# Performance work log

Hardware: AMD Instinct MI355X
Metric: run time of the kernel (lower is better)

## Reference

```python
import jax, jax.numpy as jnp
import numpy as np
from jax import lax

B, N = 4, 32768          # clouds, points per cloud (offsets are equal-sized)
CIN, COUT, S = 128, 256, 2048  # in_channels, out_channels, num_samples
EPS = 1e-5               # BatchNorm eps


def fps(xyz, npoint=S):
    """Farthest point sampling over xyz [N,3]; deterministic start index 0.
    Mirrors the torch loop: record current farthest, update min-distance, argmax."""
    n = xyz.shape[0]

    def step(carry, _):
        distance, farthest = carry
        centroid = xyz[farthest]                       # [3]
        dist = jnp.sum((xyz - centroid) ** 2, axis=1)  # [N]
        distance = jnp.minimum(distance, dist)
        new_farthest = jnp.argmax(distance).astype(jnp.int32)
        return (distance, new_farthest), farthest

    init = (jnp.full((n,), 1e10, dtype=xyz.dtype), jnp.int32(0))
    _, centroids = lax.scan(step, init, None, length=npoint)
    return centroids  # [npoint] int32


def setup_inputs():
    key = jax.random.key(0)
    k1, k2, k3 = jax.random.split(key, 3)
    coord = jax.random.normal(k1, (B * N, 3), dtype=jnp.float32)
    feat = jax.random.normal(k2, (B * N, CIN), dtype=jnp.float32)
    offset = (jnp.arange(1, B + 1, dtype=jnp.int32)) * N  # cumulative counts
    W = jax.random.normal(k3, (COUT, CIN), dtype=jnp.float32) / np.sqrt(CIN)
    gamma = jnp.ones((COUT,), dtype=jnp.float32)
    beta = jnp.zeros((COUT,), dtype=jnp.float32)
    return {"coord": coord, "feat": feat, "offset": offset,
            "W": W, "gamma": gamma, "beta": beta}


def reference(coord, feat, offset, W, gamma, beta):
    # fc -> PointBatchNorm (training-mode batch stats over B*N rows) -> ReLU
    x = feat @ W.T                                  # [B*N, COUT]
    mean = jnp.mean(x, axis=0)
    var = jnp.mean((x - mean) ** 2, axis=0)         # biased var, as torch BN
    x = (x - mean) * lax.rsqrt(var + EPS) * gamma + beta
    x = jax.nn.relu(x)

    coord_b = coord.reshape(B, N, 3)
    feat_b = x.reshape(B, N, COUT)
    idx = jax.vmap(fps)(coord_b)                    # [B, S] int32

    new_coords = jnp.take_along_axis(coord_b, idx[..., None], axis=1).reshape(B * S, 3)
    new_feats = jnp.take_along_axis(feat_b, idx[..., None], axis=1).reshape(B * S, COUT)
    new_offsets = jnp.arange(1, B + 1, dtype=jnp.int32) * S
    return new_coords, new_feats, new_offsets
```

## Files before the change

kernel.cpp:

```cpp
#include <hip/hip_runtime.h>

#define NB 4
#define NPT 32768
#define QPT 8192
#define CIN 128
#define COUT 256
#define NS 2048
#define THR 512
#define PPT 16

#define WS_G 0
#define WS_FSUM 16384
#define WS_SLOT 16512
#define WS_GSCALE 16576
#define WS_GBIAS 16832
#define WS_IDX 17088

#define OUT_COORD 0
#define OUT_FEAT 24576
#define OUT_OFFS 2121728

__global__ __launch_bounds__(THR) void fused1(
    const float* __restrict__ coord, const float* __restrict__ feat,
    float* __restrict__ wsf, int* __restrict__ wsi,
    unsigned long long* __restrict__ slots)
{
  __shared__ unsigned long long s_key[2];
  __shared__ float s_fs[4][128];

  const int bid = blockIdx.x;
  const int t = threadIdx.x;
  const bool is_fps = (bid < 32) && ((bid & 7) < 4);

  if (is_fps) {
    const int cl = bid & 3;
    const int h = bid >> 3;
    const int gbase = h * QPT;
    const float* xyz = coord + (size_t)cl * NPT * 3;
    int* idx_out = wsi + cl * NS;
    unsigned long long* slot = slots + cl * 8;

    float px[PPT], py[PPT], pz[PPT], dv[PPT];
#pragma unroll
    for (int j = 0; j < PPT; ++j) {
      int p = gbase + j * THR + t;
      px[j] = xyz[p * 3 + 0];
      py[j] = xyz[p * 3 + 1];
      pz[j] = xyz[p * 3 + 2];
      dv[j] = 1e10f;
    }
    if (t == 0) {
      if (h == 0) idx_out[0] = 0;
      s_key[0] = s_key[1] = 0ull;
    }
    float cx = xyz[0], cy = xyz[1], cz = xyz[2];
    __syncthreads();

    const int lane = t & 63;
    for (int it = 1; it < NS; ++it) {
      const int par = it & 1;
      const unsigned long long utag = (unsigned long long)it;
      float bd = -1.f;
      int bj = 0;
#pragma unroll
      for (int j = 0; j < PPT; ++j) {
        float dx = px[j] - cx, dy = py[j] - cy, dz = pz[j] - cz;
        float sx = dx * dx, sy = dy * dy, sz = dz * dz;
        asm volatile("" : "+v"(sx), "+v"(sy), "+v"(sz));
        float nd = fminf(dv[j], (sx + sy) + sz);
        dv[j] = nd;
        if (nd > bd) { bd = nd; bj = j; }
      }
      const int gidx = gbase + bj * THR + t;
      const unsigned long long tkey =
          (utag << 48) |
          ((unsigned long long)(unsigned)__float_as_int(bd) << 15) |
          (unsigned)(32767 - gidx);
      unsigned long long wkey = tkey;
#pragma unroll
      for (int o = 32; o > 0; o >>= 1) {
        unsigned long long ok = __shfl_xor(wkey, o, 64);
        wkey = ok > wkey ? ok : wkey;
      }
      if (lane == 0) atomicMax(&s_key[par], wkey);
      __syncthreads();
      const unsigned long long skey = s_key[par];
      if (tkey == skey)
        __hip_atomic_store(&slot[par * 4 + h], skey,
                           __ATOMIC_RELAXED, __HIP_MEMORY_SCOPE_AGENT);
      unsigned long long v0, v1, v2, v3;
      do {
        v0 = __hip_atomic_load(&slot[par * 4 + 0],
                               __ATOMIC_RELAXED, __HIP_MEMORY_SCOPE_AGENT);
        v1 = __hip_atomic_load(&slot[par * 4 + 1],
                               __ATOMIC_RELAXED, __HIP_MEMORY_SCOPE_AGENT);
        v2 = __hip_atomic_load(&slot[par * 4 + 2],
                               __ATOMIC_RELAXED, __HIP_MEMORY_SCOPE_AGENT);
        v3 = __hip_atomic_load(&slot[par * 4 + 3],
                               __ATOMIC_RELAXED, __HIP_MEMORY_SCOPE_AGENT);
      } while ((v0 >> 48) != utag || (v1 >> 48) != utag ||
               (v2 >> 48) != utag || (v3 >> 48) != utag);
      const unsigned long long b01 = v0 > v1 ? v0 : v1;
      const unsigned long long b23 = v2 > v3 ? v2 : v3;
      const unsigned long long best = b01 > b23 ? b01 : b23;
      const int widx = 32767 - (int)(best & 0x7fff);
      if (h == 0 && t == 0) idx_out[it] = widx;
      cx = xyz[widx * 3 + 0];
      cy = xyz[widx * 3 + 1];
      cz = xyz[widx * 3 + 2];
    }
  } else {
    const int g = (bid < 32) ? ((bid >> 3) * 4 + (bid & 7) - 4) : (bid - 16);
    if (g < 128) {
      const float* fr = feat + (size_t)g * 1024 * CIN;
      const int ti = (t & 31) * 4;
      const int tj = (t >> 5) * 8;
      float acc[4][8];
#pragma unroll
      for (int a = 0; a < 4; ++a)
#pragma unroll
        for (int b2 = 0; b2 < 8; ++b2) acc[a][b2] = 0.f;
#pragma unroll 4
      for (int r = 0; r < 1024; ++r) {
        const float* rowp = fr + r * CIN;
        float4 a4 = *(const float4*)(rowp + ti);
        float4 b4 = *(const float4*)(rowp + tj);
        float4 b5 = *(const float4*)(rowp + tj + 4);
        float av[4] = {a4.x, a4.y, a4.z, a4.w};
        float bv[8] = {b4.x, b4.y, b4.z, b4.w, b5.x, b5.y, b5.z, b5.w};
#pragma unroll
        for (int a = 0; a < 4; ++a)
#pragma unroll
          for (int b2 = 0; b2 < 8; ++b2) acc[a][b2] += av[a] * bv[b2];
      }
      float* G = wsf + WS_G;
#pragma unroll
      for (int a = 0; a < 4; ++a)
#pragma unroll
        for (int b2 = 0; b2 < 8; ++b2)
          atomicAdd(&G[(ti + a) * CIN + (tj + b2)], acc[a][b2]);
    } else {
      const int fb = g - 128;
      const size_t base = (size_t)fb * 16384;
      const int c = t & 127, rg = t >> 7;
      float s = 0.f;
      for (int r = rg; r < 16384; r += 4)
        s += feat[(base + r) * CIN + c];
      s_fs[rg][c] = s;
      __syncthreads();
      if (t < 128) {
        float v = s_fs[0][t] + s_fs[1][t] + s_fs[2][t] + s_fs[3][t];
        atomicAdd(&wsf[WS_FSUM + t], v);
      }
    }
  }
}

__global__ __launch_bounds__(128) void finalize_k(
    const float* __restrict__ W, const float* __restrict__ gamma,
    const float* __restrict__ beta, float* __restrict__ wsf)
{
  const int c = blockIdx.x, i = threadIdx.x;
  const float* G = wsf + WS_G;
  const float* fsum = wsf + WS_FSUM;
  const float* Gi = G + i * CIN;
  const float* Wc = W + c * CIN;
  float td = 0.f;
#pragma unroll 8
  for (int j = 0; j < CIN; j += 4) {
    float4 g4 = *(const float4*)(Gi + j);
    float4 w4 = *(const float4*)(Wc + j);
    td += g4.x * w4.x + g4.y * w4.y + g4.z * w4.z + g4.w * w4.w;
  }
  const float wci = Wc[i];
  float q = wci * td;
  float m = fsum[i] * wci;
#pragma unroll
  for (int o = 32; o > 0; o >>= 1) {
    q += __shfl_xor(q, o, 64);
    m += __shfl_xor(m, o, 64);
  }
  __shared__ float sq[2], sm[2];
  if ((i & 63) == 0) { sq[i >> 6] = q; sm[i >> 6] = m; }
  __syncthreads();
  if (i == 0) {
    const float inv_m = 1.f / 131072.f;
    float mean = (sm[0] + sm[1]) * inv_m;
    float e2 = (sq[0] + sq[1]) * inv_m;
    float var = e2 - mean * mean;
    float rstd = rsqrtf(var + 1e-5f);
    float gs = gamma[c] * rstd;
    wsf[WS_GSCALE + c] = gs;
    wsf[WS_GBIAS + c] = beta[c] - mean * gs;
  }
}

__global__ __launch_bounds__(256) void gather_k(
    const float* __restrict__ coord, const float* __restrict__ feat,
    const float* __restrict__ W, const float* __restrict__ wsf,
    const int* __restrict__ wsi, float* __restrict__ out)
{
  const int p = blockIdx.x, t = threadIdx.x;
  const int b = p >> 11;
  const int idx = wsi[p];
  const size_t row = (size_t)b * NPT + idx;
  __shared__ float lf[CIN];
  if (t < CIN) lf[t] = feat[row * CIN + t];
  __syncthreads();
  const float* Wc = W + t * CIN;
  float acc = 0.f;
#pragma unroll 8
  for (int k = 0; k < CIN; k += 4) {
    float4 w4 = *(const float4*)(Wc + k);
    acc += lf[k] * w4.x + lf[k + 1] * w4.y + lf[k + 2] * w4.z + lf[k + 3] * w4.w;
  }
  float y = fmaxf(fmaf(acc, wsf[WS_GSCALE + t], wsf[WS_GBIAS + t]), 0.f);
  out[OUT_FEAT + (size_t)p * COUT + t] = y;
  if (t < 3) out[OUT_COORD + p * 3 + t] = coord[row * 3 + t];
  if (p == 0 && t < 4) out[OUT_OFFS + t] = (float)((t + 1) * NS);
}

extern "C" void kernel_launch(void* const* d_in, const int* in_sizes, int n_in,
                              void* d_out, int out_size, void* d_ws, size_t ws_size,
                              hipStream_t stream)
{
  const float* coord = (const float*)d_in[0];
  const float* feat  = (const float*)d_in[1];
  const float* W     = (const float*)d_in[3];
  const float* gamma = (const float*)d_in[4];
  const float* beta  = (const float*)d_in[5];
  float* wsf = (float*)d_ws;
  int* wsi = (int*)(wsf + WS_IDX);
  unsigned long long* slots = (unsigned long long*)(wsf + WS_SLOT);
  float* out = (float*)d_out;

  hipMemsetAsync(d_ws, 0, (WS_SLOT + 64) * sizeof(float), stream);

  fused1<<<152, THR, 0, stream>>>(coord, feat, wsf, wsi, slots);
  finalize_k<<<COUT, 128, 0, stream>>>(W, gamma, beta, wsf);
  gather_k<<<NB * NS, 256, 0, stream>>>(coord, feat, W, wsf, wsi, out);
}
```

Before: 4.746 ms.

## Split FPS per cloud across two 1024-thread blocks instead of four

Each cloud's farthest-point sampling now runs on two blocks of 1024 threads, each holding half the points, instead of four blocks of 512. The per-iteration cross-block handshake polls one partner slot rather than four, which should cut global-memory spin latency on every sampling step. The GEMM and column-sum side blocks are resized to 1024 threads so the work split still matches. In exchange, each block's intra-block reduction and __syncthreads span twice as many waves, and the grid drops to 80 blocks.

```diff
diff --git a/kernel.cpp b/kernel.cpp
--- a/kernel.cpp
+++ b/kernel.cpp
@@ -2,11 +2,11 @@
 
 #define NB 4
 #define NPT 32768
-#define QPT 8192
+#define HPT 16384
 #define CIN 128
 #define COUT 256
 #define NS 2048
-#define THR 512
+#define THR 1024
 #define PPT 16
 
 #define WS_G 0
@@ -26,19 +26,19 @@
     unsigned long long* __restrict__ slots)
 {
   __shared__ unsigned long long s_key[2];
-  __shared__ float s_fs[4][128];
+  __shared__ float s_fs[8][128];
 
   const int bid = blockIdx.x;
   const int t = threadIdx.x;
-  const bool is_fps = (bid < 32) && ((bid & 7) < 4);
+  const bool is_fps = (bid < 12) && ((bid & 7) < 4);
 
   if (is_fps) {
     const int cl = bid & 3;
     const int h = bid >> 3;
-    const int gbase = h * QPT;
+    const int gbase = h * HPT;
     const float* xyz = coord + (size_t)cl * NPT * 3;
     int* idx_out = wsi + cl * NS;
-    unsigned long long* slot = slots + cl * 8;
+    unsigned long long* slot = slots + cl * 4;
 
     float px[PPT], py[PPT], pz[PPT], dv[PPT];
 #pragma unroll
@@ -86,23 +86,14 @@
       __syncthreads();
       const unsigned long long skey = s_key[par];
       if (tkey == skey)
-        __hip_atomic_store(&slot[par * 4 + h], skey,
+        __hip_atomic_store(&slot[par * 2 + h], skey,
                            __ATOMIC_RELAXED, __HIP_MEMORY_SCOPE_AGENT);
-      unsigned long long v0, v1, v2, v3;
+      unsigned long long v;
       do {
-        v0 = __hip_atomic_load(&slot[par * 4 + 0],
-                               __ATOMIC_RELAXED, __HIP_MEMORY_SCOPE_AGENT);
-        v1 = __hip_atomic_load(&slot[par * 4 + 1],
-                               __ATOMIC_RELAXED, __HIP_MEMORY_SCOPE_AGENT);
-        v2 = __hip_atomic_load(&slot[par * 4 + 2],
-                               __ATOMIC_RELAXED, __HIP_MEMORY_SCOPE_AGENT);
-        v3 = __hip_atomic_load(&slot[par * 4 + 3],
-                               __ATOMIC_RELAXED, __HIP_MEMORY_SCOPE_AGENT);
-      } while ((v0 >> 48) != utag || (v1 >> 48) != utag ||
-               (v2 >> 48) != utag || (v3 >> 48) != utag);
-      const unsigned long long b01 = v0 > v1 ? v0 : v1;
-      const unsigned long long b23 = v2 > v3 ? v2 : v3;
-      const unsigned long long best = b01 > b23 ? b01 : b23;
+        v = __hip_atomic_load(&slot[par * 2 + (1 - h)],
+                              __ATOMIC_RELAXED, __HIP_MEMORY_SCOPE_AGENT);
+      } while ((v >> 48) != utag);
+      const unsigned long long best = v > skey ? v : skey;
       const int widx = 32767 - (int)(best & 0x7fff);
       if (h == 0 && t == 0) idx_out[it] = widx;
       cx = xyz[widx * 3 + 0];
@@ -110,11 +101,12 @@
       cz = xyz[widx * 3 + 2];
     }
   } else {
-    const int g = (bid < 32) ? ((bid >> 3) * 4 + (bid & 7) - 4) : (bid - 16);
-    if (g < 128) {
-      const float* fr = feat + (size_t)g * 1024 * CIN;
-      const int ti = (t & 31) * 4;
-      const int tj = (t >> 5) * 8;
+    const int g = (bid < 8) ? (bid - 4) : (bid - 8);
+    if (g < 64) {
+      const int tt = t & 511, sub = t >> 9;
+      const float* fr = feat + ((size_t)g * 2048 + sub * 1024) * CIN;
+      const int ti = (tt & 31) * 4;
+      const int tj = (tt >> 5) * 8;
       float acc[4][8];
 #pragma unroll
       for (int a = 0; a < 4; ++a)
@@ -140,16 +132,17 @@
         for (int b2 = 0; b2 < 8; ++b2)
           atomicAdd(&G[(ti + a) * CIN + (tj + b2)], acc[a][b2]);
     } else {
-      const int fb = g - 128;
+      const int fb = g - 64;
       const size_t base = (size_t)fb * 16384;
       const int c = t & 127, rg = t >> 7;
       float s = 0.f;
-      for (int r = rg; r < 16384; r += 4)
+      for (int r = rg; r < 16384; r += 8)
         s += feat[(base + r) * CIN + c];
       s_fs[rg][c] = s;
       __syncthreads();
       if (t < 128) {
-        float v = s_fs[0][t] + s_fs[1][t] + s_fs[2][t] + s_fs[3][t];
+        float v = s_fs[0][t] + s_fs[1][t] + s_fs[2][t] + s_fs[3][t] +
+                  s_fs[4][t] + s_fs[5][t] + s_fs[6][t] + s_fs[7][t];
         atomicAdd(&wsf[WS_FSUM + t], v);
       }
     }
@@ -236,7 +229,7 @@
 
   hipMemsetAsync(d_ws, 0, (WS_SLOT + 64) * sizeof(float), stream);
 
-  fused1<<<152, THR, 0, stream>>>(coord, feat, wsf, wsi, slots);
+  fused1<<<80, THR, 0, stream>>>(coord, feat, wsf, wsi, slots);
   finalize_k<<<COUT, 128, 0, stream>>>(W, gamma, beta, wsf);
   gather_k<<<NB * NS, 256, 0, stream>>>(coord, feat, W, wsf, wsi, out);
 }
```

Measured after the change: 5.091 ms. 1.07x slower.

## Replace per-block LDS reduction with per-wave global slots in FPS

Applied to the files above, without the earlier changes.

Each FPS iteration now skips the block-level shared atomicMax and __syncthreads. Every wave instead publishes its own best key to one of 32 global slots per cloud. Each wave then polls all 32 slots at once, using one lane per slot and a wave vote, and reduces them with shuffles. This removes one barrier per iteration from the serial 2047-step loop, at the cost of more global polling traffic. The shared array is also enlarged to 64KB, which probably limits occupancy or co-residency of the blocks.

```diff
diff --git a/kernel.cpp b/kernel.cpp
--- a/kernel.cpp
+++ b/kernel.cpp
@@ -12,9 +12,9 @@
 #define WS_G 0
 #define WS_FSUM 16384
 #define WS_SLOT 16512
-#define WS_GSCALE 16576
-#define WS_GBIAS 16832
-#define WS_IDX 17088
+#define WS_GSCALE 17024
+#define WS_GBIAS 17280
+#define WS_IDX 17536
 
 #define OUT_COORD 0
 #define OUT_FEAT 24576
@@ -25,9 +25,7 @@
     float* __restrict__ wsf, int* __restrict__ wsi,
     unsigned long long* __restrict__ slots)
 {
-  __shared__ unsigned long long s_key[2];
-  __shared__ float s_fs[4][128];
-
+  __shared__ float smem[16384];
   const int bid = blockIdx.x;
   const int t = threadIdx.x;
   const bool is_fps = (bid < 32) && ((bid & 7) < 4);
@@ -38,7 +36,7 @@
     const int gbase = h * QPT;
     const float* xyz = coord + (size_t)cl * NPT * 3;
     int* idx_out = wsi + cl * NS;
-    unsigned long long* slot = slots + cl * 8;
+    unsigned long long* slot = slots + cl * 64;
 
     float px[PPT], py[PPT], pz[PPT], dv[PPT];
 #pragma unroll
@@ -49,17 +47,15 @@
       pz[j] = xyz[p * 3 + 2];
       dv[j] = 1e10f;
     }
-    if (t == 0) {
-      if (h == 0) idx_out[0] = 0;
-      s_key[0] = s_key[1] = 0ull;
-    }
+    if (h == 0 && t == 0) idx_out[0] = 0;
     float cx = xyz[0], cy = xyz[1], cz = xyz[2];
-    __syncthreads();
-
     const int lane = t & 63;
+    const int wslot = h * 8 + (t >> 6);
+
     for (int it = 1; it < NS; ++it) {
       const int par = it & 1;
       const unsigned long long utag = (unsigned long long)it;
+      unsigned long long* slotp = slot + par * 32;
       float bd = -1.f;
       int bj = 0;
 #pragma unroll
@@ -72,38 +68,29 @@
         if (nd > bd) { bd = nd; bj = j; }
       }
       const int gidx = gbase + bj * THR + t;
-      const unsigned long long tkey =
+      unsigned long long wkey =
           (utag << 48) |
           ((unsigned long long)(unsigned)__float_as_int(bd) << 15) |
           (unsigned)(32767 - gidx);
-      unsigned long long wkey = tkey;
 #pragma unroll
       for (int o = 32; o > 0; o >>= 1) {
         unsigned long long ok = __shfl_xor(wkey, o, 64);
         wkey = ok > wkey ? ok : wkey;
       }
-      if (lane == 0) atomicMax(&s_key[par], wkey);
-      __syncthreads();
-      const unsigned long long skey = s_key[par];
-      if (tkey == skey)
-        __hip_atomic_store(&slot[par * 4 + h], skey,
+      if (lane == 0)
+        __hip_atomic_store(&slotp[wslot], wkey,
                            __ATOMIC_RELAXED, __HIP_MEMORY_SCOPE_AGENT);
-      unsigned long long v0, v1, v2, v3;
+      unsigned long long v;
       do {
-        v0 = __hip_atomic_load(&slot[par * 4 + 0],
-                               __ATOMIC_RELAXED, __HIP_MEMORY_SCOPE_AGENT);
-        v1 = __hip_atomic_load(&slot[par * 4 + 1],
-                               __ATOMIC_RELAXED, __HIP_MEMORY_SCOPE_AGENT);
-        v2 = __hip_atomic_load(&slot[par * 4 + 2],
-                               __ATOMIC_RELAXED, __HIP_MEMORY_SCOPE_AGENT);
-        v3 = __hip_atomic_load(&slot[par * 4 + 3],
-                               __ATOMIC_RELAXED, __HIP_MEMORY_SCOPE_AGENT);
-      } while ((v0 >> 48) != utag || (v1 >> 48) != utag ||
-               (v2 >> 48) != utag || (v3 >> 48) != utag);
-      const unsigned long long b01 = v0 > v1 ? v0 : v1;
-      const unsigned long long b23 = v2 > v3 ? v2 : v3;
-      const unsigned long long best = b01 > b23 ? b01 : b23;
-      const int widx = 32767 - (int)(best & 0x7fff);
+        v = __hip_atomic_load(&slotp[lane & 31],
+                              __ATOMIC_RELAXED, __HIP_MEMORY_SCOPE_AGENT);
+      } while (!__all((int)((v >> 48) == utag)));
+#pragma unroll
+      for (int o = 16; o > 0; o >>= 1) {
+        unsigned long long ov = __shfl_xor(v, o, 64);
+        v = ov > v ? ov : v;
+      }
+      const int widx = 32767 - (int)(v & 0x7fff);
       if (h == 0 && t == 0) idx_out[it] = widx;
       cx = xyz[widx * 3 + 0];
       cy = xyz[widx * 3 + 1];
@@ -140,6 +127,7 @@
         for (int b2 = 0; b2 < 8; ++b2)
           atomicAdd(&G[(ti + a) * CIN + (tj + b2)], acc[a][b2]);
     } else {
+      float (*s_fs)[128] = (float (*)[128])smem;
       const int fb = g - 128;
       const size_t base = (size_t)fb * 16384;
       const int c = t & 127, rg = t >> 7;
@@ -234,7 +222,7 @@
   unsigned long long* slots = (unsigned long long*)(wsf + WS_SLOT);
   float* out = (float*)d_out;
 
-  hipMemsetAsync(d_ws, 0, (WS_SLOT + 64) * sizeof(float), stream);
+  hipMemsetAsync(d_ws, 0, (WS_SLOT + 512) * sizeof(float), stream);
 
   fused1<<<152, THR, 0, stream>>>(coord, feat, wsf, wsi, slots);
   finalize_k<<<COUT, 128, 0, stream>>>(W, gamma, beta, wsf);
```

After: 7.646 ms. +61.1%, slower.
